# Performance work log

Hardware: AMD Instinct MI355X
Metric: run time of the kernel (lower is better)

The kernel has to match this reference:

```python
import jax, jax.numpy as jnp
import numpy as np

B, T, D_ENC, V, E, H = 16, 2000, 512, 1024, 256, 2
P, J = 640, 640
BLANK = 0


def _lin(k, i, o):
    s = 1.0 / np.sqrt(i)
    return jax.random.uniform(k, (i, o), jnp.float32, -s, s)


def setup_inputs() -> dict:
    key = jax.random.key(0)
    ks = jax.random.split(key, 12)
    return {
        "encoder_out": jax.random.normal(ks[0], (B, T, D_ENC), jnp.float32),
        "features_len": jnp.full((B,), T, jnp.int32),
        "targets": jax.random.randint(ks[1], (B, T), 0, V),
        "W_enc": _lin(ks[2], D_ENC, V), "b_enc": jnp.zeros((V,), jnp.float32),
        "emb": jax.random.normal(ks[3], (V, E), jnp.float32) * 0.1,
        "W_p1": _lin(ks[4], H * E, P), "b_p1": jnp.zeros((P,), jnp.float32),
        "W_p2": _lin(ks[5], P, P), "b_p2": jnp.zeros((P,), jnp.float32),
        "W_po": _lin(ks[6], P, V), "b_po": jnp.zeros((V,), jnp.float32),
        "W_j1": _lin(ks[7], V, J), "b_j1": jnp.zeros((J,), jnp.float32),
        "W_j2": _lin(ks[8], J, V), "b_j2": jnp.zeros((V,), jnp.float32),
    }


def _viterbi_context(targets):
    # c[0] = blank; c[t] = targets[t-1] if targets[t-1] != blank else c[t-1]
    # == last non-blank target at a position strictly before t, else blank.
    t_idx = jnp.arange(targets.shape[1])
    pos = jnp.where(targets != BLANK, t_idx[None, :], -1)
    last = jax.lax.cummax(pos, axis=1)                                   # [B,T] last non-blank idx <= t
    last = jnp.pad(last[:, :-1], ((0, 0), (1, 0)), constant_values=-1)   # strictly < t
    gathered = jnp.take_along_axis(targets, jnp.maximum(last, 0), axis=1)
    return jnp.where(last >= 0, gathered, BLANK)


def _extend_context_history(context):
    # stack [c, shift(c,1), ...] along last dim, padding with blank
    hist = [context]
    for _ in range(H - 1):
        hist.append(jnp.pad(hist[-1][:, :-1], ((0, 0), (1, 0)), constant_values=BLANK))
    return jnp.stack(hist, axis=-1)  # [B,T,H]


def reference(encoder_out, features_len, targets, W_enc, b_enc, emb,
              W_p1, b_p1, W_p2, b_p2, W_po, b_po, W_j1, b_j1, W_j2, b_j2):
    # encoder head
    enc = encoder_out @ W_enc + b_enc                    # [B,T,V]
    enc_lens = features_len.astype(jnp.int32)
    enc_log_probs = jax.nn.log_softmax(enc, axis=2)

    # viterbi context + predictor (dropout is identity in eval/reference)
    ctx = _extend_context_history(_viterbi_context(targets))   # [B,T,H]
    a = emb[ctx]                                                # [B,T,H,E]
    a = a.reshape(*a.shape[:-2], H * E)                         # [B,T,H*E]
    a = jnp.tanh(a @ W_p1 + b_p1)
    a = jnp.tanh(a @ W_p2 + b_p2)
    pred = a @ W_po + b_po                                      # [B,T,V]
    pred_log_probs = jax.nn.log_softmax(pred, axis=2)

    # joint network on enc + pred
    h = jnp.tanh((enc + pred) @ W_j1 + b_j1)
    logits = h @ W_j2 + b_j2
    log_probs = jax.nn.log_softmax(logits, axis=2)
    return log_probs, pred_log_probs, enc_log_probs, enc_lens
```

## Files before the change

### kernel.cpp

```cpp
#include <hip/hip_runtime.h>
#include <math.h>

typedef unsigned short ushort_t;
typedef unsigned int uint_t;

#define BB 16
#define TT 2000
#define DENC 512
#define VV 1024
#define EE 256
#define PP 640
#define PPAD 768
#define MM (BB * TT)

typedef __attribute__((ext_vector_type(8))) short bf16x8;
typedef __attribute__((ext_vector_type(4))) float f32x4;

__device__ __forceinline__ ushort_t f2bf(float x) {
    union { float f; uint_t u; } v; v.f = x;
    uint_t r = v.u + 0x7fffu + ((v.u >> 16) & 1u);
    return (ushort_t)(r >> 16);
}

__device__ __forceinline__ void async_ld16(const ushort_t* g, ushort_t* l) {
    __builtin_amdgcn_global_load_lds(
        (const __attribute__((address_space(1))) void*)g,
        (__attribute__((address_space(3))) void*)l, 16, 0, 0);
}

#define NB_CVT  16000
#define B_TR    16000
#define NB_TR   3152
#define B_EMB   (B_TR + NB_TR)
#define NB_EMB  256
#define B_PAD   (B_EMB + NB_EMB)
#define NB_PAD  34
#define B_MISC  (B_PAD + NB_PAD)
#define B_CTX   (B_MISC + 1)
#define NB_PREP (B_CTX + BB)

__global__ __launch_bounds__(256) void prep_kernel(
    const float* __restrict__ encoder_out, const int* __restrict__ features_len,
    const int* __restrict__ targets,
    const float* __restrict__ W_enc, const float* __restrict__ W_p1,
    const float* __restrict__ W_p2,  const float* __restrict__ W_po,
    const float* __restrict__ W_j1,  const float* __restrict__ W_j2,
    const float* __restrict__ b_p1,  const float* __restrict__ b_p2,
    const float* __restrict__ b_j1,  const float* __restrict__ emb,
    ushort_t* __restrict__ Abuf,
    ushort_t* __restrict__ WTenc, ushort_t* __restrict__ WTp1,
    ushort_t* __restrict__ WTp2,  ushort_t* __restrict__ WTpo,
    ushort_t* __restrict__ WTj1,  ushort_t* __restrict__ WTj2,
    ushort_t* __restrict__ embB,
    float* __restrict__ bp1p, float* __restrict__ bp2p, float* __restrict__ bj1p,
    int* __restrict__ ctx0, int* __restrict__ ctx1, float* __restrict__ out_lens) {
    const int blk = blockIdx.x;
    const int tid = threadIdx.x;

    if (blk < NB_CVT) {
        size_t i = ((size_t)blk * 256 + tid) * 4;
        float4 v = *(const float4*)(encoder_out + i);
        ushort_t o[4] = {f2bf(v.x), f2bf(v.y), f2bf(v.z), f2bf(v.w)};
        *(uint2*)(Abuf + i) = *(uint2*)o;
        return;
    }
    if (blk < B_EMB) {
        int t = blk - B_TR;
        const float* W; ushort_t* WT; int K, N, base;
        if (t < 512)       { W = W_enc; WT = WTenc; K = 512;  N = 1024; base = 0; }
        else if (t < 832)  { W = W_p1;  WT = WTp1;  K = 512;  N = 640;  base = 512; }
        else if (t < 1232) { W = W_p2;  WT = WTp2;  K = 640;  N = 640;  base = 832; }
        else if (t < 1872) { W = W_po;  WT = WTpo;  K = 640;  N = 1024; base = 1232; }
        else if (t < 2512) { W = W_j1;  WT = WTj1;  K = 1024; N = 640;  base = 1872; }
        else               { W = W_j2;  WT = WTj2;  K = 640;  N = 1024; base = 2512; }
        t -= base;
        const int tilesN = N / 32;
        const int n0 = (t % tilesN) * 32, k0 = (t / tilesN) * 32;
        __shared__ float sm[32][33];
        const int tx = tid & 31, ty0 = tid >> 5;
        #pragma unroll
        for (int i = 0; i < 4; ++i) {
            int ty = ty0 + i * 8;
            sm[ty][tx] = W[(size_t)(k0 + ty) * N + n0 + tx];
        }
        __syncthreads();
        #pragma unroll
        for (int i = 0; i < 4; ++i) {
            int ty = ty0 + i * 8;
            WT[(size_t)(n0 + ty) * K + k0 + tx] = f2bf(sm[tx][ty]);
        }
        return;
    }
    if (blk < B_PAD) {
        int t = blk - B_EMB;
        size_t i = ((size_t)t * 256 + tid) * 4;
        float4 v = *(const float4*)(emb + i);
        ushort_t o[4] = {f2bf(v.x), f2bf(v.y), f2bf(v.z), f2bf(v.w)};
        *(uint2*)(embB + i) = *(uint2*)o;
        return;
    }
    if (blk < B_MISC) {
        int t = blk - B_PAD;
        ushort_t* dst; size_t off;
        if (t < 8)       { dst = WTp1 + (size_t)640 * 512;  off = (size_t)t * 8192; }
        else if (t < 18) { dst = WTp2 + (size_t)640 * 640;  off = (size_t)(t - 8) * 8192; }
        else             { dst = WTj1 + (size_t)640 * 1024; off = (size_t)(t - 18) * 8192; }
        uint4 z = {0, 0, 0, 0};
        ushort_t* p = dst + off + tid * 32;
        #pragma unroll
        for (int i = 0; i < 4; ++i) *(uint4*)(p + i * 8) = z;
        return;
    }
    if (blk < B_CTX) {
        for (int t = tid; t < PPAD; t += 256) {
            bp1p[t] = (t < PP) ? b_p1[t] : 0.f;
            bp2p[t] = (t < PP) ? b_p2[t] : 0.f;
            bj1p[t] = (t < PP) ? b_j1[t] : 0.f;
        }
        if (tid < BB) out_lens[tid] = (float)features_len[tid];
        return;
    }
    {
        const int b = blk - B_CTX;
        __shared__ int tg[2048];
        __shared__ int cc[2048];
        __shared__ int wl[4];
        const int* row = targets + b * TT;
        for (int t = tid; t < 2048; t += 256) tg[t] = (t < TT) ? row[t] : 0;
        __syncthreads();
        const int lane = tid & 63, wv = tid >> 6;
        const int base = tid * 8;
        int lastIdx = -1;
        #pragma unroll
        for (int i = 0; i < 8; ++i) { if (tg[base + i] != 0) lastIdx = base + i; }
        int incl = lastIdx;
        #pragma unroll
        for (int o = 1; o < 64; o <<= 1) {
            int u = __shfl_up(incl, o, 64);
            if (lane >= o) incl = max(incl, u);
        }
        if (lane == 63) wl[wv] = incl;
        __syncthreads();
        int excl = -1;
        for (int w = 0; w < 4; ++w) if (w < wv) excl = max(excl, wl[w]);
        int u = __shfl_up(incl, 1, 64);
        if (lane > 0) excl = max(excl, u);
        int cur = excl;
        #pragma unroll
        for (int i = 0; i < 8; ++i) {
            int idx = base + i;
            cc[idx] = (cur >= 0) ? tg[cur] : 0;
            if (tg[idx] != 0) cur = idx;
        }
        __syncthreads();
        for (int t = tid; t < TT; t += 256) {
            ctx0[b * TT + t] = cc[t];
            ctx1[b * TT + t] = t ? cc[t - 1] : 0;
        }
    }
}

__device__ __forceinline__ void stage_half(const ushort_t* __restrict__ X, int xBase,
                                           int lda, int kt, int h, ushort_t* region,
                                           int tid) {
    const int wb = tid & ~63;
    #pragma unroll
    for (int s = 0; s < 2; ++s) {
        const int c  = s * 512 + tid;
        const int rH = c >> 3;
        const int k8 = (c & 7) ^ (rH & 7);
        const ushort_t* g = X + (size_t)(xBase + h * 128 + rH) * lda + kt + k8 * 8;
        ushort_t* l = region + ((size_t)(h * 1024 + s * 512 + wb)) * 8;
        async_ld16(g, l);
    }
}

__device__ __forceinline__ void stage_g(const ushort_t* b0, const ushort_t* b1,
                                        int kt, int h, int s, ushort_t* region, int tid) {
    const int wb = tid & ~63;
    const int c  = s * 512 + tid;
    const int rH = c >> 3;
    const int k8 = (c & 7) ^ (rH & 7);
    const ushort_t* base = (kt < 256) ? (b0 + kt) : (b1 + (kt - 256));
    async_ld16(base + k8 * 8, region + ((size_t)(h * 1024 + s * 512 + wb)) * 8);
}

template<int OMODE, bool GATHER>
__global__ __launch_bounds__(512, 2) void gemm256_kernel(
    const ushort_t* __restrict__ A, const ushort_t* __restrict__ BT,
    const float* __restrict__ bias, void* __restrict__ Cout,
    const float* __restrict__ addIn, ushort_t* __restrict__ sumOut,
    const ushort_t* __restrict__ embB, const int* __restrict__ ctx0,
    const int* __restrict__ ctx1,
    int N, int K, int lda, int ldc, int GX) {
    extern __shared__ __align__(16) ushort_t smem[];
    ushort_t* A0 = smem;
    ushort_t* B0 = smem + 16384;
    ushort_t* A1 = smem + 32768;
    ushort_t* B1 = smem + 49152;

    const int nwg = gridDim.x;
    const int orig = blockIdx.x;
    const int q8 = nwg >> 3, r8 = nwg & 7;
    const int xcd = orig & 7, slot = orig >> 3;
    const int wgid = (xcd < r8 ? xcd * (q8 + 1) : r8 * (q8 + 1) + (xcd - r8) * q8) + slot;
    const int bx = wgid % GX, by = wgid / GX;

    const int tid = threadIdx.x;
    const int lane = tid & 63;
    const int ln = lane & 15, quad = lane >> 4;
    const int wave = tid >> 6;
    const int wr = wave >> 2, wc = wave & 3;
    const int rowBase = by * 256, colBase = bx * 256;
    const int NT = K >> 6;

    const ushort_t* g0[2][2];
    const ushort_t* g1[2][2];
    if (GATHER) {
        #pragma unroll
        for (int h = 0; h < 2; ++h)
            #pragma unroll
            for (int s = 0; s < 2; ++s) {
                int rH = (s * 512 + tid) >> 3;
                int row = rowBase + h * 128 + rH;
                g0[h][s] = embB + (size_t)ctx0[row] * EE;
                g1[h][s] = embB + (size_t)ctx1[row] * EE;
            }
    }

    f32x4 acc[4][2][4] = {};

    if (GATHER) {
        stage_g(g0[0][0], g1[0][0], 0, 0, 0, A0, tid);
        stage_g(g0[0][1], g1[0][1], 0, 0, 1, A0, tid);
        stage_g(g0[1][0], g1[1][0], 0, 1, 0, A0, tid);
        stage_g(g0[1][1], g1[1][1], 0, 1, 1, A0, tid);
    } else {
        stage_half(A, rowBase, lda, 0, 0, A0, tid);
        stage_half(A, rowBase, lda, 0, 1, A0, tid);
    }
    stage_half(BT, colBase, K, 0,  0, B0, tid);
    stage_half(BT, colBase, K, 0,  1, B0, tid);
    stage_half(BT, colBase, K, 64, 0, B1, tid);
    stage_half(BT, colBase, K, 64, 1, B1, tid);
    asm volatile("s_waitcnt vmcnt(4)" ::: "memory");
    __builtin_amdgcn_s_barrier();

    for (int t = 0; t < NT; ++t) {
        const int cur = t & 1;
        const char* cA = (const char*)(cur ? A1 : A0);
        const char* cB = (const char*)(cur ? B1 : B0);
        ushort_t* oA  = cur ? A0 : A1;
        ushort_t* cBw = cur ? B1 : B0;
        const int ktA = (t + 1 < NT ? t + 1 : NT - 1) * 64;
        const int ktB = (t + 2 < NT ? t + 2 : NT - 1) * 64;

        bf16x8 bfr[4][2];
        #pragma unroll
        for (int q = 0; q < 4; ++q) {
            if (q == 0) {
                #pragma unroll
                for (int n = 0; n < 4; ++n)
                    #pragma unroll
                    for (int ks = 0; ks < 2; ++ks) {
                        int off = (wc * 64 + n * 16 + ln) * 128 + ks * 64 + quad * 16;
                        off ^= (ln & 7) << 4;
                        bfr[n][ks] = *(const bf16x8*)(cB + off);
                    }
            }
            bf16x8 afr[2][2];
            #pragma unroll
            for (int m = 0; m < 2; ++m)
                #pragma unroll
                for (int ks = 0; ks < 2; ++ks) {
                    int off = (wr * 128 + q * 32 + m * 16 + ln) * 128 + ks * 64 + quad * 16;
                    off ^= (ln & 7) << 4;
                    afr[m][ks] = *(const bf16x8*)(cA + off);
                }
            if (q == 0) {
                if (GATHER) { stage_g(g0[0][0], g1[0][0], ktA, 0, 0, oA, tid);
                              stage_g(g0[0][1], g1[0][1], ktA, 0, 1, oA, tid); }
                else        stage_half(A, rowBase, lda, ktA, 0, oA, tid);
            } else if (q == 1) {
                if (GATHER) { stage_g(g0[1][0], g1[1][0], ktA, 1, 0, oA, tid);
                              stage_g(g0[1][1], g1[1][1], ktA, 1, 1, oA, tid); }
                else        stage_half(A, rowBase, lda, ktA, 1, oA, tid);
            } else if (q == 2) {
                stage_half(BT, colBase, K, ktB, 0, cBw, tid);
            } else {
                stage_half(BT, colBase, K, ktB, 1, cBw, tid);
            }

            __builtin_amdgcn_s_barrier();
            __builtin_amdgcn_s_setprio(1);
            #pragma unroll
            for (int m = 0; m < 2; ++m)
                #pragma unroll
                for (int n = 0; n < 4; ++n)
                    #pragma unroll
                    for (int ks = 0; ks < 2; ++ks)
                        acc[q][m][n] = __builtin_amdgcn_mfma_f32_16x16x32_bf16(
                            afr[m][ks], bfr[n][ks], acc[q][m][n], 0, 0, 0);
            __builtin_amdgcn_s_setprio(0);
            if (q == 3)
                asm volatile("s_waitcnt vmcnt(4)" ::: "memory");
            __builtin_amdgcn_s_barrier();
        }
    }

    float bv[4];
    #pragma unroll
    for (int n = 0; n < 4; ++n) bv[n] = bias[colBase + wc * 64 + n * 16 + ln];

    #pragma unroll
    for (int q = 0; q < 4; ++q)
        #pragma unroll
        for (int m = 0; m < 2; ++m)
            #pragma unroll
            for (int rr = 0; rr < 4; ++rr) {
                const size_t row = (size_t)(rowBase + wr * 128 + q * 32 + m * 16 + quad * 4 + rr);
                #pragma unroll
                for (int n = 0; n < 4; ++n) {
                    const int col = colBase + wc * 64 + n * 16 + ln;
                    const size_t idx = row * (size_t)ldc + col;
                    float v = acc[q][m][n][rr] + bv[n];
                    if (OMODE == 0) {
                        ((float*)Cout)[idx] = v;
                    } else if (OMODE == 1) {
                        ((ushort_t*)Cout)[idx] = f2bf(tanhf(v));
                    } else {
                        ((float*)Cout)[idx] = v;
                        sumOut[idx] = f2bf(v + addIn[idx]);
                    }
                }
            }
}

__global__ __launch_bounds__(256) void logsoftmax_kernel(float* __restrict__ x) {
    const int wave = threadIdx.x >> 6, lane = threadIdx.x & 63;
    const size_t base = ((size_t)blockIdx.x * 4 + wave) * VV;

    float4 v[4];
    #pragma unroll
    for (int i = 0; i < 4; ++i)
        v[i] = *(const float4*)&x[base + i * 256 + lane * 4];

    float m = fmaxf(fmaxf(v[0].x, v[0].y), fmaxf(v[0].z, v[0].w));
    #pragma unroll
    for (int i = 1; i < 4; ++i)
        m = fmaxf(m, fmaxf(fmaxf(v[i].x, v[i].y), fmaxf(v[i].z, v[i].w)));
    #pragma unroll
    for (int o = 1; o < 64; o <<= 1) m = fmaxf(m, __shfl_xor(m, o, 64));

    float s = 0.f;
    #pragma unroll
    for (int i = 0; i < 4; ++i)
        s += expf(v[i].x - m) + expf(v[i].y - m) + expf(v[i].z - m) + expf(v[i].w - m);
    #pragma unroll
    for (int o = 1; o < 64; o <<= 1) s += __shfl_xor(s, o, 64);

    const float lse = logf(s) + m;
    #pragma unroll
    for (int i = 0; i < 4; ++i) {
        v[i].x -= lse; v[i].y -= lse; v[i].z -= lse; v[i].w -= lse;
        *(float4*)&x[base + i * 256 + lane * 4] = v[i];
    }
}

extern "C" void kernel_launch(void* const* d_in, const int* in_sizes, int n_in,
                              void* d_out, int out_size, void* d_ws, size_t ws_size,
                              hipStream_t stream) {
    const float* encoder_out  = (const float*)d_in[0];
    const int*   features_len = (const int*)  d_in[1];
    const int*   targets      = (const int*)  d_in[2];
    const float* W_enc = (const float*)d_in[3];
    const float* b_enc = (const float*)d_in[4];
    const float* emb   = (const float*)d_in[5];
    const float* W_p1  = (const float*)d_in[6];
    const float* b_p1  = (const float*)d_in[7];
    const float* W_p2  = (const float*)d_in[8];
    const float* b_p2  = (const float*)d_in[9];
    const float* W_po  = (const float*)d_in[10];
    const float* b_po  = (const float*)d_in[11];
    const float* W_j1  = (const float*)d_in[12];
    const float* b_j1  = (const float*)d_in[13];
    const float* W_j2  = (const float*)d_in[14];
    const float* b_j2  = (const float*)d_in[15];

    float* out = (float*)d_out;
    const size_t BTV = (size_t)MM * VV;
    float* out_logits = out;
    float* out_pred   = out + BTV;
    float* out_enc    = out + 2 * BTV;
    float* out_lens   = out + 3 * BTV;

    char* ws = (char*)d_ws;
    int*      ctx0  = (int*)ws;
    int*      ctx1  = (int*)(ws + 128000);
    size_t off = 256000;
    ushort_t* embB  = (ushort_t*)(ws + off); off += (size_t)VV * EE * 2;
    ushort_t* WTenc = (ushort_t*)(ws + off); off += (size_t)VV * DENC * 2;
    ushort_t* WTp1  = (ushort_t*)(ws + off); off += (size_t)PPAD * DENC * 2;
    ushort_t* WTp2  = (ushort_t*)(ws + off); off += (size_t)PPAD * PP * 2;
    ushort_t* WTpo  = (ushort_t*)(ws + off); off += (size_t)VV * PP * 2;
    ushort_t* WTj1  = (ushort_t*)(ws + off); off += (size_t)PPAD * VV * 2;
    ushort_t* WTj2  = (ushort_t*)(ws + off); off += (size_t)VV * PP * 2;
    float*    bp1p  = (float*)(ws + off); off += PPAD * 4;
    float*    bp2p  = (float*)(ws + off); off += PPAD * 4;
    float*    bj1p  = (float*)(ws + off); off += PPAD * 4;
    ushort_t* h1    = (ushort_t*)(ws + off); off += (size_t)MM * PPAD * 2;
    ushort_t* Abuf  = (ushort_t*)(ws + off); off += (size_t)MM * DENC * 2;
    ushort_t* h2    = (ushort_t*)(ws + off);
    ushort_t* sumb  = h1;

    hipFuncSetAttribute((const void*)&gemm256_kernel<1, true>,
                        hipFuncAttributeMaxDynamicSharedMemorySize, 131072);
    hipFuncSetAttribute((const void*)&gemm256_kernel<0, false>,
                        hipFuncAttributeMaxDynamicSharedMemorySize, 131072);
    hipFuncSetAttribute((const void*)&gemm256_kernel<1, false>,
                        hipFuncAttributeMaxDynamicSharedMemorySize, 131072);
    hipFuncSetAttribute((const void*)&gemm256_kernel<2, false>,
                        hipFuncAttributeMaxDynamicSharedMemorySize, 131072);

    prep_kernel<<<NB_PREP, 256, 0, stream>>>(
        encoder_out, features_len, targets,
        W_enc, W_p1, W_p2, W_po, W_j1, W_j2,
        b_p1, b_p2, b_j1, emb,
        Abuf, WTenc, WTp1, WTp2, WTpo, WTj1, WTj2,
        embB, bp1p, bp2p, bj1p, ctx0, ctx1, out_lens);

    gemm256_kernel<1, true><<<(PPAD/256)*(MM/256), 512, 131072, stream>>>(
        nullptr, WTp1, bp1p, h1, nullptr, nullptr, embB, ctx0, ctx1,
        PPAD, DENC, 0, PPAD, PPAD/256);

    gemm256_kernel<0, false><<<(VV/256)*(MM/256), 512, 131072, stream>>>(
        Abuf, WTenc, b_enc, out_enc, nullptr, nullptr, nullptr, nullptr, nullptr,
        VV, DENC, DENC, VV, VV/256);

    gemm256_kernel<1, false><<<(PPAD/256)*(MM/256), 512, 131072, stream>>>(
        h1, WTp2, bp2p, h2, nullptr, nullptr, nullptr, nullptr, nullptr,
        PPAD, PP, PPAD, PPAD, PPAD/256);

    gemm256_kernel<2, false><<<(VV/256)*(MM/256), 512, 131072, stream>>>(
        h2, WTpo, b_po, out_pred, out_enc, sumb, nullptr, nullptr, nullptr,
        VV, PP, PPAD, VV, VV/256);

    gemm256_kernel<1, false><<<(PPAD/256)*(MM/256), 512, 131072, stream>>>(
        sumb, WTj1, bj1p, h2, nullptr, nullptr, nullptr, nullptr, nullptr,
        PPAD, VV, VV, PPAD, PPAD/256);

    gemm256_kernel<0, false><<<(VV/256)*(MM/256), 512, 131072, stream>>>(
        h2, WTj2, b_j2, out_logits, nullptr, nullptr, nullptr, nullptr, nullptr,
        VV, PP, PPAD, VV, VV/256);

    logsoftmax_kernel<<<3 * MM / 4, 256, 0, stream>>>(out);
}
```

Measured before the change: 952.4 us.

## Fuse log-softmax into full-row V-output GEMMs with 64-row tiles

Replaces the three N=1024 GEMMs plus the separate log-softmax pass with a new kernel where each block computes a full 64x1024 output row tile and does the row max/sum reduction in registers and LDS before writing log-probs. The goal is to remove the extra read/write round trip of the 3*MM*V float outputs through the standalone softmax kernel. The cost is a narrow 64-row M tile with low A reuse per block, a larger LDS footprint, and an extra raw encoder buffer written and read to form the joint input sum.

```diff
diff --git a/kernel.cpp b/kernel.cpp
--- a/kernel.cpp
+++ b/kernel.cpp
@@ -189,7 +189,6 @@
 __global__ __launch_bounds__(512, 2) void gemm256_kernel(
     const ushort_t* __restrict__ A, const ushort_t* __restrict__ BT,
     const float* __restrict__ bias, void* __restrict__ Cout,
-    const float* __restrict__ addIn, ushort_t* __restrict__ sumOut,
     const ushort_t* __restrict__ embB, const int* __restrict__ ctx0,
     const int* __restrict__ ctx1,
     int N, int K, int lda, int ldc, int GX) {
@@ -324,47 +323,151 @@
                     const int col = colBase + wc * 64 + n * 16 + ln;
                     const size_t idx = row * (size_t)ldc + col;
                     float v = acc[q][m][n][rr] + bv[n];
-                    if (OMODE == 0) {
-                        ((float*)Cout)[idx] = v;
-                    } else if (OMODE == 1) {
-                        ((ushort_t*)Cout)[idx] = f2bf(tanhf(v));
-                    } else {
-                        ((float*)Cout)[idx] = v;
-                        sumOut[idx] = f2bf(v + addIn[idx]);
-                    }
+                    ((ushort_t*)Cout)[idx] = f2bf(tanhf(v));
                 }
             }
 }
 
-__global__ __launch_bounds__(256) void logsoftmax_kernel(float* __restrict__ x) {
-    const int wave = threadIdx.x >> 6, lane = threadIdx.x & 63;
-    const size_t base = ((size_t)blockIdx.x * 4 + wave) * VV;
-
-    float4 v[4];
+__device__ __forceinline__ void stage64(const ushort_t* __restrict__ A,
+                                        const ushort_t* __restrict__ BT,
+                                        int row0, int lda, int K, int kt,
+                                        ushort_t* Ab, ushort_t* Bb, int tid) {
+    const int wb = tid & ~63;
+    #pragma unroll
+    for (int s = 0; s < 8; ++s) {
+        const int c = s * 512 + tid;
+        const int rB = c >> 2, p = c & 3;
+        const int k8 = p ^ (rB & 3);
+        async_ld16(BT + (size_t)rB * K + kt + k8 * 8, Bb + (s * 512 + wb) * 8);
+    }
+    if (tid < 256) {
+        const int rA = tid >> 2, p = tid & 3;
+        const int k8 = p ^ (rA & 3);
+        async_ld16(A + (size_t)(row0 + rA) * lda + kt + k8 * 8, Ab + wb * 8);
+    }
+}
+
+template<int SMODE>
+__global__ __launch_bounds__(512, 2) void gemm_sm_kernel(
+    const ushort_t* __restrict__ A, const ushort_t* __restrict__ BT,
+    const float* __restrict__ bias, float* __restrict__ outLP,
+    float* __restrict__ rawBuf,
+    ushort_t* __restrict__ sumOut,
+    int K, int lda) {
+    extern __shared__ __align__(16) ushort_t smem[];
+    ushort_t* Ab0 = smem;
+    ushort_t* Ab1 = smem + 2048;
+    ushort_t* Bb0 = smem + 4096;
+    ushort_t* Bb1 = smem + 4096 + 32768;
+    float* redmax = (float*)(smem + 4096 + 65536);
+    float* redsum = redmax + 512;
+
+    const int tid = threadIdx.x;
+    const int lane = tid & 63;
+    const int ln = lane & 15, quad = lane >> 4;
+    const int w = tid >> 6;
+    const int row0 = blockIdx.x * 64;
+    const int NT = K >> 5;
+
+    f32x4 acc[4][8] = {};
+
+    stage64(A, BT, row0, lda, K, 0, Ab0, Bb0, tid);
+    asm volatile("s_waitcnt vmcnt(0)" ::: "memory");
+    __builtin_amdgcn_s_barrier();
+
+    for (int t = 0; t < NT; ++t) {
+        const char* cAb = (const char*)((t & 1) ? Ab1 : Ab0);
+        const char* cBb = (const char*)((t & 1) ? Bb1 : Bb0);
+        if (t + 1 < NT)
+            stage64(A, BT, row0, lda, K, (t + 1) << 5,
+                    (t & 1) ? Ab0 : Ab1, (t & 1) ? Bb0 : Bb1, tid);
+
+        bf16x8 a[4], b[8];
+        #pragma unroll
+        for (int i = 0; i < 4; ++i) {
+            int row = i * 16 + ln;
+            int off = row * 64 + ((quad ^ (row & 3)) << 4);
+            a[i] = *(const bf16x8*)(cAb + off);
+        }
+        #pragma unroll
+        for (int n = 0; n < 8; ++n) {
+            int row = w * 128 + n * 16 + ln;
+            int off = row * 64 + ((quad ^ (row & 3)) << 4);
+            b[n] = *(const bf16x8*)(cBb + off);
+        }
+        __builtin_amdgcn_s_setprio(1);
+        #pragma unroll
+        for (int i = 0; i < 4; ++i)
+            #pragma unroll
+            for (int n = 0; n < 8; ++n)
+                acc[i][n] = __builtin_amdgcn_mfma_f32_16x16x32_bf16(
+                    a[i], b[n], acc[i][n], 0, 0, 0);
+        __builtin_amdgcn_s_setprio(0);
+        if (t + 1 < NT)
+            asm volatile("s_waitcnt vmcnt(0)" ::: "memory");
+        __builtin_amdgcn_s_barrier();
+    }
+
+    float bv[8];
+    #pragma unroll
+    for (int n = 0; n < 8; ++n) bv[n] = bias[w * 128 + n * 16 + ln];
     #pragma unroll
     for (int i = 0; i < 4; ++i)
-        v[i] = *(const float4*)&x[base + i * 256 + lane * 4];
-
-    float m = fmaxf(fmaxf(v[0].x, v[0].y), fmaxf(v[0].z, v[0].w));
-    #pragma unroll
-    for (int i = 1; i < 4; ++i)
-        m = fmaxf(m, fmaxf(fmaxf(v[i].x, v[i].y), fmaxf(v[i].z, v[i].w)));
-    #pragma unroll
-    for (int o = 1; o < 64; o <<= 1) m = fmaxf(m, __shfl_xor(m, o, 64));
-
-    float s = 0.f;
+        #pragma unroll
+        for (int n = 0; n < 8; ++n)
+            acc[i][n] += bv[n];
+
     #pragma unroll
     for (int i = 0; i < 4; ++i)
-        s += expf(v[i].x - m) + expf(v[i].y - m) + expf(v[i].z - m) + expf(v[i].w - m);
-    #pragma unroll
-    for (int o = 1; o < 64; o <<= 1) s += __shfl_xor(s, o, 64);
-
-    const float lse = logf(s) + m;
-    #pragma unroll
-    for (int i = 0; i < 4; ++i) {
-        v[i].x -= lse; v[i].y -= lse; v[i].z -= lse; v[i].w -= lse;
-        *(float4*)&x[base + i * 256 + lane * 4] = v[i];
-    }
+        #pragma unroll
+        for (int rr = 0; rr < 4; ++rr) {
+            float m = acc[i][0][rr];
+            #pragma unroll
+            for (int n = 1; n < 8; ++n) m = fmaxf(m, acc[i][n][rr]);
+            #pragma unroll
+            for (int o = 1; o < 16; o <<= 1) m = fmaxf(m, __shfl_xor(m, o, 64));
+            if (ln == 0) redmax[w * 64 + i * 16 + quad * 4 + rr] = m;
+        }
+    __syncthreads();
+
+    float Mr[4][4];
+    #pragma unroll
+    for (int i = 0; i < 4; ++i)
+        #pragma unroll
+        for (int rr = 0; rr < 4; ++rr) {
+            const int row = i * 16 + quad * 4 + rr;
+            float m = redmax[row];
+            #pragma unroll
+            for (int ww = 1; ww < 8; ++ww) m = fmaxf(m, redmax[ww * 64 + row]);
+            Mr[i][rr] = m;
+            float s = 0.f;
+            #pragma unroll
+            for (int n = 0; n < 8; ++n) s += expf(acc[i][n][rr] - m);
+            #pragma unroll
+            for (int o = 1; o < 16; o <<= 1) s += __shfl_xor(s, o, 64);
+            if (ln == 0) redsum[w * 64 + row] = s;
+        }
+    __syncthreads();
+
+    #pragma unroll
+    for (int i = 0; i < 4; ++i)
+        #pragma unroll
+        for (int rr = 0; rr < 4; ++rr) {
+            const int row = i * 16 + quad * 4 + rr;
+            float S = 0.f;
+            #pragma unroll
+            for (int ww = 0; ww < 8; ++ww) S += redsum[ww * 64 + row];
+            const float lse = logf(S) + Mr[i][rr];
+            const size_t gr = (size_t)(row0 + row) * VV;
+            #pragma unroll
+            for (int n = 0; n < 8; ++n) {
+                const int col = w * 128 + n * 16 + ln;
+                const float v = acc[i][n][rr];
+                if (SMODE == 1) rawBuf[gr + col] = v;
+                if (SMODE == 2) sumOut[gr + col] = f2bf(v + rawBuf[gr + col]);
+                outLP[gr + col] = v - lse;
+            }
+        }
 }
 
 extern "C" void kernel_launch(void* const* d_in, const int* in_sizes, int n_in,
@@ -410,17 +513,20 @@
     float*    bj1p  = (float*)(ws + off); off += PPAD * 4;
     ushort_t* h1    = (ushort_t*)(ws + off); off += (size_t)MM * PPAD * 2;
     ushort_t* Abuf  = (ushort_t*)(ws + off); off += (size_t)MM * DENC * 2;
-    ushort_t* h2    = (ushort_t*)(ws + off);
+    ushort_t* h2    = (ushort_t*)(ws + off); off += (size_t)MM * PPAD * 2;
+    float*    encraw= (float*)(ws + off);
     ushort_t* sumb  = h1;
 
     hipFuncSetAttribute((const void*)&gemm256_kernel<1, true>,
-                        hipFuncAttributeMaxDynamicSharedMemorySize, 131072);
-    hipFuncSetAttribute((const void*)&gemm256_kernel<0, false>,
                         hipFuncAttributeMaxDynamicSharedMemorySize, 131072);
     hipFuncSetAttribute((const void*)&gemm256_kernel<1, false>,
                         hipFuncAttributeMaxDynamicSharedMemorySize, 131072);
-    hipFuncSetAttribute((const void*)&gemm256_kernel<2, false>,
-                        hipFuncAttributeMaxDynamicSharedMemorySize, 131072);
+    hipFuncSetAttribute((const void*)&gemm_sm_kernel<0>,
+                        hipFuncAttributeMaxDynamicSharedMemorySize, 143360);
+    hipFuncSetAttribute((const void*)&gemm_sm_kernel<1>,
+                        hipFuncAttributeMaxDynamicSharedMemorySize, 143360);
+    hipFuncSetAttribute((const void*)&gemm_sm_kernel<2>,
+                        hipFuncAttributeMaxDynamicSharedMemorySize, 143360);
 
     prep_kernel<<<NB_PREP, 256, 0, stream>>>(
         encoder_out, features_len, targets,
@@ -430,28 +536,23 @@
         embB, bp1p, bp2p, bj1p, ctx0, ctx1, out_lens);
 
     gemm256_kernel<1, true><<<(PPAD/256)*(MM/256), 512, 131072, stream>>>(
-        nullptr, WTp1, bp1p, h1, nullptr, nullptr, embB, ctx0, ctx1,
+        nullptr, WTp1, bp1p, h1, embB, ctx0, ctx1,
         PPAD, DENC, 0, PPAD, PPAD/256);
 
-    gemm256_kernel<0, false><<<(VV/256)*(MM/256), 512, 131072, stream>>>(
-        Abuf, WTenc, b_enc, out_enc, nullptr, nullptr, nullptr, nullptr, nullptr,
-        VV, DENC, DENC, VV, VV/256);
+    gemm_sm_kernel<1><<<MM/64, 512, 143360, stream>>>(
+        Abuf, WTenc, b_enc, out_enc, encraw, nullptr, DENC, DENC);
 
     gemm256_kernel<1, false><<<(PPAD/256)*(MM/256), 512, 131072, stream>>>(
-        h1, WTp2, bp2p, h2, nullptr, nullptr, nullptr, nullptr, nullptr,
+        h1, WTp2, bp2p, h2, nullptr, nullptr, nullptr,
         PPAD, PP, PPAD, PPAD, PPAD/256);
 
-    gemm256_kernel<2, false><<<(VV/256)*(MM/256), 512, 131072, stream>>>(
-        h2, WTpo, b_po, out_pred, out_enc, sumb, nullptr, nullptr, nullptr,
-        VV, PP, PPAD, VV, VV/256);
+    gemm_sm_kernel<2><<<MM/64, 512, 143360, stream>>>(
+        h2, WTpo, b_po, out_pred, encraw, sumb, PP, PPAD);
 
     gemm256_kernel<1, false><<<(PPAD/256)*(MM/256), 512, 131072, stream>>>(
-        sumb, WTj1, bj1p, h2, nullptr, nullptr, nullptr, nullptr, nullptr,
+        sumb, WTj1, bj1p, h2, nullptr, nullptr, nullptr,
         PPAD, VV, VV, PPAD, PPAD/256);
 
-    gemm256_kernel<0, false><<<(VV/256)*(MM/256), 512, 131072, stream>>>(
-        h2, WTj2, b_j2, out_logits, nullptr, nullptr, nullptr, nullptr, nullptr,
-        VV, PP, PPAD, VV, VV/256);
-
-    logsoftmax_kernel<<<3 * MM / 4, 256, 0, stream>>>(out);
-}
+    gemm_sm_kernel<0><<<MM/64, 512, 143360, stream>>>(
+        h2, WTj2, b_j2, out_logits, nullptr, nullptr, PP, PPAD);
+}
```

Result: slower. 1.018 ms (+6.9%).
